# Kernel tuning notes

Hardware: AMD Instinct MI355X
Metric: run time of the kernel (lower is better)

## Reference

```python
import jax, jax.numpy as jnp
import numpy as np
from jax import lax

D_MODEL = 384
D_STATE = 16
D_CONV = 4
EXPAND = 2
D_INNER = EXPAND * D_MODEL            # 768
DT_RANK = int(np.ceil(D_INNER / 16))  # 48
B_SZ, L_SEQ = 8, 1024
LN_EPS = 1e-5


def setup_inputs() -> dict:
    key = jax.random.key(0)
    ks = jax.random.split(key, 10)
    x = jax.random.normal(ks[0], (B_SZ, L_SEQ, D_MODEL), dtype=jnp.float32)
    ln_g = jnp.ones((D_MODEL,), jnp.float32)
    ln_b = jnp.zeros((D_MODEL,), jnp.float32)
    in_proj_w = jax.random.normal(ks[1], (2 * D_INNER, D_MODEL), jnp.float32) * (D_MODEL ** -0.5)
    conv_w = jax.random.normal(ks[2], (D_INNER, 1, D_CONV), jnp.float32) * (D_CONV ** -0.5)
    conv_b = jax.random.normal(ks[3], (D_INNER,), jnp.float32) * 0.01
    x_proj_w = jax.random.normal(ks[4], (DT_RANK + 2 * D_STATE, D_INNER), jnp.float32) * (D_INNER ** -0.5)
    dt_std = DT_RANK ** -0.5
    dt_proj_w = jax.random.uniform(ks[5], (D_INNER, DT_RANK), jnp.float32, -dt_std, dt_std)
    dt_proj_b = jax.random.normal(ks[6], (D_INNER,), jnp.float32) * 0.01
    A_log = jnp.log(jnp.tile(jnp.arange(1, D_STATE + 1, dtype=jnp.float32), (D_INNER, 1)))
    D_param = jnp.ones((D_INNER,), jnp.float32)
    out_proj_w = jax.random.normal(ks[7], (D_MODEL, D_INNER), jnp.float32) * (D_INNER ** -0.5)
    return {"x": x, "ln_g": ln_g, "ln_b": ln_b, "in_proj_w": in_proj_w,
            "conv_w": conv_w, "conv_b": conv_b, "x_proj_w": x_proj_w,
            "dt_proj_w": dt_proj_w, "dt_proj_b": dt_proj_b, "A_log": A_log,
            "D_param": D_param, "out_proj_w": out_proj_w}


def _selective_scan(u, delta, A, Bm, Cm):
    # u, delta: (B,L,Din); A: (Din,N); Bm, Cm: (B,L,N)
    dA = jnp.exp(delta[..., None] * A)                 # (B,L,Din,N)
    dBu = (delta * u)[..., None] * Bm[:, :, None, :]   # (B,L,Din,N)
    dA_t = jnp.moveaxis(dA, 1, 0)                      # (L,B,Din,N)
    dBu_t = jnp.moveaxis(dBu, 1, 0)
    C_t = jnp.moveaxis(Cm, 1, 0)                       # (L,B,N)

    def step(h, inp):
        dA_s, dBu_s, c_s = inp
        h = dA_s * h + dBu_s                           # (B,Din,N)
        y = jnp.einsum('bdn,bn->bd', h, c_s)
        return h, y

    h0 = jnp.zeros((u.shape[0], u.shape[2], A.shape[1]), u.dtype)
    _, ys = lax.scan(step, h0, (dA_t, dBu_t, C_t))
    return jnp.moveaxis(ys, 0, 1)                      # (B,L,Din)


def reference(x, ln_g, ln_b, in_proj_w, conv_w, conv_b, x_proj_w,
              dt_proj_w, dt_proj_b, A_log, D_param, out_proj_w):
    residual = x
    # LayerNorm
    mu = jnp.mean(x, axis=-1, keepdims=True)
    var = jnp.var(x, axis=-1, keepdims=True)
    xn = (x - mu) * lax.rsqrt(var + LN_EPS) * ln_g + ln_b
    # in_proj and split
    xz = xn @ in_proj_w.T                              # (B,L,2*Din)
    xh, z = jnp.split(xz, 2, axis=-1)
    # causal depthwise conv1d (torch pads both sides then truncates to L)
    xc = lax.conv_general_dilated(
        jnp.moveaxis(xh, 1, 2), conv_w, (1,), [(D_CONV - 1, 0)],
        feature_group_count=D_INNER,
        dimension_numbers=('NCH', 'OIH', 'NCH')) + conv_b[None, :, None]
    u = jax.nn.silu(jnp.moveaxis(xc, 1, 2))            # (B,L,Din)
    # SSM input-dependent params
    xpo = u @ x_proj_w.T                               # (B,L,dt_rank+2N)
    dlow, Bm, Cm = jnp.split(xpo, [DT_RANK, DT_RANK + D_STATE], axis=-1)
    delta = jax.nn.softplus(dlow @ dt_proj_w.T + dt_proj_b)
    A = -jnp.exp(A_log)
    y = _selective_scan(u, delta, A, Bm, Cm)
    y = y + u * D_param
    y = y * jax.nn.silu(z)
    out = y @ out_proj_w.T
    return residual + out
```

## Files before the change

kernel.cpp:

```cpp
#include <hip/hip_runtime.h>
#include <math.h>

#define DMODEL 384
#define DIN 768
#define NST 16
#define DTR 48
#define BSZ 8
#define LSEQ 1024
#define NROWS (BSZ*LSEQ)
#define XPO_W (DTR + 2*NST)
#define CL 32
#define NC (LSEQ/CL)
#define CSEG 32

typedef __attribute__((ext_vector_type(8))) short bf16x8;
typedef __attribute__((ext_vector_type(4))) float f32x4;

__device__ __forceinline__ unsigned short f2bf(float x) {
  unsigned int u = __float_as_uint(x);
  unsigned int r = u + 0x7fffu + ((u >> 16) & 1u);
  return (unsigned short)(r >> 16);
}
__device__ __forceinline__ float bf2f(unsigned short h) {
  return __uint_as_float(((unsigned int)h) << 16);
}
__device__ __forceinline__ unsigned int pk2(float a, float b) {
  return (unsigned int)f2bf(a) | ((unsigned int)f2bf(b) << 16);
}

__device__ __forceinline__ void gll16(const void* g, void* l) {
  __builtin_amdgcn_global_load_lds(
      (const __attribute__((address_space(1))) void*)g,
      (__attribute__((address_space(3))) void*)l, 16, 0, 0);
}

__device__ __forceinline__ void split_one(const float* src, int ldsrc, int R, int C,
    unsigned short* dh, unsigned short* dl, int Cpad, int i) {
  int r = i / Cpad, c = i - r * Cpad;
  float v = (r < R && c < C) ? src[(size_t)r*ldsrc + c] : 0.f;
  unsigned short hv = f2bf(v);
  dh[i] = hv;
  dl[i] = f2bf(v - bf2f(hv));
}
#define N_INW (1536*384)
#define N_XW  (128*768)
#define N_DTW (768*64)
#define N_OW  (384*768)
#define NWBLK ((N_INW+N_XW+N_DTW+N_OW)/256)
__global__ __launch_bounds__(256) void prep_kernel(
    const float* __restrict__ inw, const float* __restrict__ xw,
    const float* __restrict__ dtw, const float* __restrict__ ow,
    unsigned short* inw_h, unsigned short* inw_l,
    unsigned short* xw_h, unsigned short* xw_l,
    unsigned short* dtw_h, unsigned short* dtw_l,
    unsigned short* ow_h, unsigned short* ow_l,
    const float* __restrict__ x, const float* __restrict__ g,
    const float* __restrict__ b,
    unsigned short* __restrict__ xh, unsigned short* __restrict__ xl) {
  if (blockIdx.x < NWBLK) {
    int i = blockIdx.x * 256 + threadIdx.x;
    if (i < N_INW) { split_one(inw, 384, 1536, 384, inw_h, inw_l, 384, i); return; }
    i -= N_INW;
    if (i < N_XW)  { split_one(xw, 768, 80, 768, xw_h, xw_l, 768, i); return; }
    i -= N_XW;
    if (i < N_DTW) { split_one(dtw, 48, 768, 48, dtw_h, dtw_l, 64, i); return; }
    i -= N_DTW;
    split_one(ow, 768, 384, 768, ow_h, ow_l, 768, i);
    return;
  }
  int row = (blockIdx.x - NWBLK) * 4 + (threadIdx.x >> 6);
  int lane = threadIdx.x & 63;
  const float* xr = x + (size_t)row * DMODEL;
  float v[6];
  float s = 0.f, ss = 0.f;
#pragma unroll
  for (int i = 0; i < 6; ++i) { v[i] = xr[lane + i*64]; s += v[i]; ss += v[i]*v[i]; }
#pragma unroll
  for (int off = 32; off; off >>= 1) { s += __shfl_xor(s, off); ss += __shfl_xor(ss, off); }
  float mu = s * (1.f / DMODEL);
  float var = ss * (1.f / DMODEL) - mu * mu;
  float inv = rsqrtf(var + 1e-5f);
#pragma unroll
  for (int i = 0; i < 6; ++i) {
    int c = lane + i*64;
    float o = (v[i] - mu) * inv * g[c] + b[c];
    unsigned short hv = f2bf(o);
    xh[(size_t)row*DMODEL + c] = hv;
    xl[(size_t)row*DMODEL + c] = f2bf(o - bf2f(hv));
  }
}

template<int EPI>
__global__ __launch_bounds__(256, 2) void gemm_mfma(
    const unsigned short* __restrict__ Ah, const unsigned short* __restrict__ Al, int lda,
    const unsigned short* __restrict__ Bh, const unsigned short* __restrict__ Bl, int ldb,
    float* __restrict__ C, int ldc, size_t strideS,
    const float* __restrict__ bias,
    int T) {
  __shared__ unsigned short lds[2][4][4096];
  int tid = threadIdx.x;
  int lane = tid & 63, wid = tid >> 6;
  int wm = wid >> 1, wn = wid & 1;

  unsigned nwg = gridDim.x * gridDim.y;
  unsigned bid = blockIdx.y * gridDim.x + blockIdx.x;
  unsigned cpx = nwg >> 3;
  unsigned sw = (bid & 7) * cpx + (bid >> 3);
  unsigned bx = sw % gridDim.x, by = sw / gridDim.x;
  int m0 = by * 128, n0 = bx * 128;
  C += (size_t)blockIdx.z * strideS;
  size_t kofs = (size_t)blockIdx.z * T * 32;

  f32x4 acc[4][4];
#pragma unroll
  for (int i = 0; i < 4; ++i)
#pragma unroll
    for (int j = 0; j < 4; ++j) acc[i][j] = (f32x4){0.f, 0.f, 0.f, 0.f};

  int kgl = lane >> 4, rl = lane & 15;

  int c0 = wid*128 + lane;
  int c1 = wid*128 + 64 + lane;
  int r0 = c0 & 127, kg0 = c0 >> 7;
  int r1 = c1 & 127, kg1 = c1 >> 7;

#define STAGE(bf, kt) do { \
    size_t ga0 = (size_t)(m0 + r0) * lda + (kt) + kg0*8 + kofs; \
    size_t gb0 = (size_t)(n0 + r0) * ldb + (kt) + kg0*8 + kofs; \
    size_t ga1 = (size_t)(m0 + r1) * lda + (kt) + kg1*8 + kofs; \
    size_t gb1 = (size_t)(n0 + r1) * ldb + (kt) + kg1*8 + kofs; \
    gll16(Ah + ga0, &lds[bf][0][(wid*128)*8]); \
    gll16(Al + ga0, &lds[bf][1][(wid*128)*8]); \
    gll16(Bh + gb0, &lds[bf][2][(wid*128)*8]); \
    gll16(Bl + gb0, &lds[bf][3][(wid*128)*8]); \
    gll16(Ah + ga1, &lds[bf][0][(wid*128+64)*8]); \
    gll16(Al + ga1, &lds[bf][1][(wid*128+64)*8]); \
    gll16(Bh + gb1, &lds[bf][2][(wid*128+64)*8]); \
    gll16(Bl + gb1, &lds[bf][3][(wid*128+64)*8]); \
  } while (0)

  STAGE(0, 0);
  asm volatile("s_waitcnt vmcnt(0)" ::: "memory");
  __builtin_amdgcn_s_barrier();

  int cur = 0;
  for (int t = 0; t < T; ++t) {
    if (t + 1 < T) {
      STAGE(cur ^ 1, (t + 1) << 5);
    }
    asm volatile("" ::: "memory");
    bf16x8 ah[4], al[4], bh[4], bl[4];
#pragma unroll
    for (int mi = 0; mi < 4; ++mi) {
      int cell = kgl*128 + wm*64 + mi*16 + rl;
      ah[mi] = *reinterpret_cast<const bf16x8*>(&lds[cur][0][cell*8]);
      al[mi] = *reinterpret_cast<const bf16x8*>(&lds[cur][1][cell*8]);
    }
#pragma unroll
    for (int ni = 0; ni < 4; ++ni) {
      int cell = kgl*128 + wn*64 + ni*16 + rl;
      bh[ni] = *reinterpret_cast<const bf16x8*>(&lds[cur][2][cell*8]);
      bl[ni] = *reinterpret_cast<const bf16x8*>(&lds[cur][3][cell*8]);
    }
#pragma unroll
    for (int mi = 0; mi < 4; ++mi)
#pragma unroll
      for (int ni = 0; ni < 4; ++ni) {
        acc[mi][ni] = __builtin_amdgcn_mfma_f32_16x16x32_bf16(ah[mi], bh[ni], acc[mi][ni], 0, 0, 0);
        acc[mi][ni] = __builtin_amdgcn_mfma_f32_16x16x32_bf16(al[mi], bh[ni], acc[mi][ni], 0, 0, 0);
        acc[mi][ni] = __builtin_amdgcn_mfma_f32_16x16x32_bf16(ah[mi], bl[ni], acc[mi][ni], 0, 0, 0);
      }
    asm volatile("s_waitcnt vmcnt(0)" ::: "memory");
    __builtin_amdgcn_s_barrier();
    cur ^= 1;
  }
#undef STAGE

#pragma unroll
  for (int mi = 0; mi < 4; ++mi)
#pragma unroll
    for (int ni = 0; ni < 4; ++ni)
#pragma unroll
      for (int j = 0; j < 4; ++j) {
        int m = m0 + wm*64 + mi*16 + (lane>>4)*4 + j;
        int n = n0 + wn*64 + ni*16 + (lane&15);
        float v = acc[mi][ni][j];
        if (EPI == 0) {
          C[(size_t)m*ldc + n] = v;
        } else if (EPI == 2) {
          v += bias[n];
          v = (v > 20.f) ? v : log1pf(__expf(v));
          C[(size_t)m*ldc + n] = v;
        }
      }
}

__global__ __launch_bounds__(256) void reduce_xproj(
    const float* __restrict__ P, float* __restrict__ xpo,
    unsigned short* __restrict__ dh, unsigned short* __restrict__ dl) {
  int idx = blockIdx.x * 256 + threadIdx.x;
  int m = idx >> 7, n = idx & 127;
  float v = 0.f;
#pragma unroll
  for (int s = 0; s < 4; ++s) v += P[(size_t)s * NROWS * 128 + idx];
  if (n < XPO_W) xpo[(size_t)m * XPO_W + n] = v;
  if (n < 64) {
    unsigned short hv = f2bf(v);
    dh[(size_t)m*64 + n] = hv;
    dl[(size_t)m*64 + n] = f2bf(v - bf2f(hv));
  }
}

__global__ __launch_bounds__(256) void reduce_out(
    const float* __restrict__ P, const float* __restrict__ x, float* __restrict__ out) {
  int i = blockIdx.x * 256 + threadIdx.x;
  const size_t S = (size_t)NROWS*DMODEL;
  out[i] = x[i] + ((P[i] + P[i + S]) + (P[i + 2*S] + P[i + 3*S]));
}

__global__ __launch_bounds__(256) void conv_silu_kernel(
    const float* __restrict__ xz, const float* __restrict__ w,
    const float* __restrict__ cb,
    unsigned short* __restrict__ uh, unsigned short* __restrict__ ul) {
  int d = blockIdx.x * 256 + threadIdx.x;
  int l0 = blockIdx.y * CSEG;
  int b = blockIdx.z;
  float xv[CSEG + 3];
#pragma unroll
  for (int i = 0; i < CSEG + 3; ++i) {
    int l = l0 + i - 3;
    xv[i] = (l >= 0) ? xz[((size_t)b*LSEQ + l) * (2*DIN) + d] : 0.f;
  }
  float w0 = w[d*4], w1 = w[d*4+1], w2 = w[d*4+2], w3 = w[d*4+3];
  float cbv = cb[d];
#pragma unroll
  for (int i = 0; i < CSEG; ++i) {
    float acc = cbv;
    acc = fmaf(xv[i],     w0, acc);
    acc = fmaf(xv[i + 1], w1, acc);
    acc = fmaf(xv[i + 2], w2, acc);
    acc = fmaf(xv[i + 3], w3, acc);
    float s = acc / (1.f + __expf(-acc));
    size_t idx = ((size_t)b*LSEQ + l0 + i) * DIN + d;
    unsigned short hv = f2bf(s);
    uh[idx] = hv;
    ul[idx] = f2bf(s - bf2f(hv));
  }
}

__global__ __launch_bounds__(256) void scan_pass1(
    const float* __restrict__ delta,
    const unsigned short* __restrict__ uh,
    const float* __restrict__ xpo, const float* __restrict__ A_log,
    unsigned short* __restrict__ carryA, unsigned short* __restrict__ carryH) {
  int d = blockIdx.x * 256 + threadIdx.x;
  int c = blockIdx.y, b = blockIdx.z;
  float A[16];
  {
    const float4* al = reinterpret_cast<const float4*>(A_log + (size_t)d * NST);
#pragma unroll
    for (int i = 0; i < 4; ++i) {
      float4 t = al[i];
      A[4*i+0] = -__expf(t.x); A[4*i+1] = -__expf(t.y);
      A[4*i+2] = -__expf(t.z); A[4*i+3] = -__expf(t.w);
    }
  }
  float h[16], ap[16];
#pragma unroll
  for (int n = 0; n < 16; ++n) { h[n] = 0.f; ap[n] = 1.f; }
  const float* dp = delta + ((size_t)b*LSEQ + c*CL) * DIN + d;
  const unsigned short* uhp = uh + ((size_t)b*LSEQ + c*CL) * DIN + d;
  const float* bp = xpo   + ((size_t)b*LSEQ + c*CL) * XPO_W + DTR;
  for (int l = 0; l < CL; ++l) {
    float dv = dp[(size_t)l*DIN];
    float uv = bf2f(uhp[(size_t)l*DIN]);
    float du = dv * uv;
    float Bv[16];
    {
      const float4* b4 = reinterpret_cast<const float4*>(bp + (size_t)l*XPO_W);
#pragma unroll
      for (int i = 0; i < 4; ++i) {
        float4 t = b4[i];
        Bv[4*i+0] = t.x; Bv[4*i+1] = t.y; Bv[4*i+2] = t.z; Bv[4*i+3] = t.w;
      }
    }
#pragma unroll
    for (int n = 0; n < 16; ++n) {
      float a = __expf(dv * A[n]);
      ap[n] *= a;
      h[n] = fmaf(a, h[n], du * Bv[n]);
    }
  }
  size_t ci = (((size_t)b*NC + c) * DIN + d) * NST;
  uint4* ca = reinterpret_cast<uint4*>(carryA + ci);
  uint4* ch = reinterpret_cast<uint4*>(carryH + ci);
  ca[0] = make_uint4(pk2(ap[0],ap[1]), pk2(ap[2],ap[3]), pk2(ap[4],ap[5]), pk2(ap[6],ap[7]));
  ca[1] = make_uint4(pk2(ap[8],ap[9]), pk2(ap[10],ap[11]), pk2(ap[12],ap[13]), pk2(ap[14],ap[15]));
  ch[0] = make_uint4(pk2(h[0],h[1]), pk2(h[2],h[3]), pk2(h[4],h[5]), pk2(h[6],h[7]));
  ch[1] = make_uint4(pk2(h[8],h[9]), pk2(h[10],h[11]), pk2(h[12],h[13]), pk2(h[14],h[15]));
}

__global__ __launch_bounds__(256) void scan_mid(
    const unsigned short* __restrict__ carryA, unsigned short* __restrict__ carryH) {
  int idx = blockIdx.x * 256 + threadIdx.x;
  int b = idx / (DIN*NST);
  int rem = idx - b * DIN*NST;
  float h = 0.f;
#pragma unroll
  for (int c = 0; c < NC; ++c) {
    size_t i = ((size_t)b*NC + c) * (DIN*NST) + rem;
    float a = bf2f(carryA[i]);
    float e = bf2f(carryH[i]);
    carryH[i] = f2bf(h);
    h = fmaf(a, h, e);
  }
}

__global__ __launch_bounds__(256) void scan_pass2(
    const float* __restrict__ delta,
    const unsigned short* __restrict__ uh,
    const float* __restrict__ xpo, const float* __restrict__ xz,
    const float* __restrict__ A_log, const float* __restrict__ Dp,
    const unsigned short* __restrict__ carryH,
    unsigned short* __restrict__ yh, unsigned short* __restrict__ yl) {
  int d = blockIdx.x * 256 + threadIdx.x;
  int c = blockIdx.y, b = blockIdx.z;
  float A[16];
  {
    const float4* al = reinterpret_cast<const float4*>(A_log + (size_t)d * NST);
#pragma unroll
    for (int i = 0; i < 4; ++i) {
      float4 t = al[i];
      A[4*i+0] = -__expf(t.x); A[4*i+1] = -__expf(t.y);
      A[4*i+2] = -__expf(t.z); A[4*i+3] = -__expf(t.w);
    }
  }
  float h[16];
  size_t ci = (((size_t)b*NC + c) * DIN + d) * NST;
  {
    const uint4* ch4 = reinterpret_cast<const uint4*>(carryH + ci);
    uint4 t0 = ch4[0], t1 = ch4[1];
    h[0] = bf2f(t0.x & 0xffff); h[1] = bf2f(t0.x >> 16);
    h[2] = bf2f(t0.y & 0xffff); h[3] = bf2f(t0.y >> 16);
    h[4] = bf2f(t0.z & 0xffff); h[5] = bf2f(t0.z >> 16);
    h[6] = bf2f(t0.w & 0xffff); h[7] = bf2f(t0.w >> 16);
    h[8] = bf2f(t1.x & 0xffff); h[9] = bf2f(t1.x >> 16);
    h[10] = bf2f(t1.y & 0xffff); h[11] = bf2f(t1.y >> 16);
    h[12] = bf2f(t1.z & 0xffff); h[13] = bf2f(t1.z >> 16);
    h[14] = bf2f(t1.w & 0xffff); h[15] = bf2f(t1.w >> 16);
  }
  float Dd = Dp[d];
  const float* dp = delta + ((size_t)b*LSEQ + c*CL) * DIN + d;
  const unsigned short* uhp = uh + ((size_t)b*LSEQ + c*CL) * DIN + d;
  const float* bp = xpo   + ((size_t)b*LSEQ + c*CL) * XPO_W + DTR;
  const float* zp = xz    + ((size_t)b*LSEQ + c*CL) * (2*DIN) + DIN + d;
  size_t yi0 = ((size_t)b*LSEQ + c*CL) * DIN + d;
  for (int l = 0; l < CL; ++l) {
    float dv = dp[(size_t)l*DIN];
    float uv = bf2f(uhp[(size_t)l*DIN]);
    float du = dv * uv;
    float Bv[16], Cv[16];
    {
      const float4* b4 = reinterpret_cast<const float4*>(bp + (size_t)l*XPO_W);
#pragma unroll
      for (int i = 0; i < 4; ++i) {
        float4 t = b4[i];
        Bv[4*i+0] = t.x; Bv[4*i+1] = t.y; Bv[4*i+2] = t.z; Bv[4*i+3] = t.w;
        float4 tc = b4[i+4];
        Cv[4*i+0] = tc.x; Cv[4*i+1] = tc.y; Cv[4*i+2] = tc.z; Cv[4*i+3] = tc.w;
      }
    }
    float p = 0.f;
#pragma unroll
    for (int n = 0; n < 16; ++n) {
      float a = __expf(dv * A[n]);
      h[n] = fmaf(a, h[n], du * Bv[n]);
      p = fmaf(h[n], Cv[n], p);
    }
    float z = zp[(size_t)l*(2*DIN)];
    float sz = z / (1.f + __expf(-z));
    float yv = fmaf(uv, Dd, p) * sz;
    unsigned short hv = f2bf(yv);
    yh[yi0 + (size_t)l*DIN] = hv;
    yl[yi0 + (size_t)l*DIN] = f2bf(yv - bf2f(hv));
  }
}

extern "C" void kernel_launch(void* const* d_in, const int* in_sizes, int n_in,
                              void* d_out, int out_size, void* d_ws, size_t ws_size,
                              hipStream_t stream) {
  const float* x          = (const float*)d_in[0];
  const float* ln_g       = (const float*)d_in[1];
  const float* ln_b       = (const float*)d_in[2];
  const float* in_proj_w  = (const float*)d_in[3];
  const float* conv_w     = (const float*)d_in[4];
  const float* conv_b     = (const float*)d_in[5];
  const float* x_proj_w   = (const float*)d_in[6];
  const float* dt_proj_w  = (const float*)d_in[7];
  const float* dt_proj_b  = (const float*)d_in[8];
  const float* A_log      = (const float*)d_in[9];
  const float* D_param    = (const float*)d_in[10];
  const float* out_proj_w = (const float*)d_in[11];

  char* w = (char*)d_ws;
  unsigned short* xn_h  = (unsigned short*)w;
  unsigned short* xn_l  = xn_h + (size_t)NROWS*DMODEL;
  unsigned short* dlow_h = (unsigned short*)w;
  unsigned short* dlow_l = dlow_h + (size_t)NROWS*64;
  unsigned short* carryA = (unsigned short*)w;
  unsigned short* carryH = carryA + (size_t)BSZ*NC*DIN*NST;
  char* p = w + (size_t)NROWS*DMODEL*4;
  float* xz = (float*)p;              p += (size_t)NROWS*2*DIN*4;
  unsigned short* u_h = (unsigned short*)p;
  unsigned short* u_l = u_h + (size_t)NROWS*DIN;      p += (size_t)NROWS*DIN*4;
  float* xpo = (float*)p;             p += (size_t)NROWS*XPO_W*4;
  float* delta = (float*)p;           p += (size_t)NROWS*DIN*4;
  unsigned short* inw_h = (unsigned short*)delta;
  unsigned short* inw_l = inw_h + (size_t)1536*384;
  unsigned short* xw_h  = inw_l + (size_t)1536*384;
  unsigned short* xw_l  = xw_h + (size_t)128*768;
  unsigned short* y2_h = (unsigned short*)p;
  unsigned short* y2_l = y2_h + (size_t)NROWS*DIN;
  float* xpart = (float*)p;           p += (size_t)NROWS*DIN*4;
  unsigned short* dtw_h = (unsigned short*)p;
  unsigned short* dtw_l = dtw_h + (size_t)768*64;
  unsigned short* ow_h  = dtw_l + (size_t)768*64;
  unsigned short* ow_l  = ow_h + (size_t)384*768;
  float* opart = xz;

  prep_kernel<<<NWBLK + NROWS/4, 256, 0, stream>>>(
      in_proj_w, x_proj_w, dt_proj_w, out_proj_w,
      inw_h, inw_l, xw_h, xw_l, dtw_h, dtw_l, ow_h, ow_l,
      x, ln_g, ln_b, xn_h, xn_l);

  gemm_mfma<0><<<dim3(12, 64, 1), 256, 0, stream>>>(xn_h, xn_l, DMODEL, inw_h, inw_l, DMODEL,
      xz, 2*DIN, 0, nullptr, 12);

  conv_silu_kernel<<<dim3(DIN/256, LSEQ/CSEG, BSZ), 256, 0, stream>>>(
      xz, conv_w, conv_b, u_h, u_l);

  gemm_mfma<0><<<dim3(1, 64, 4), 256, 0, stream>>>(u_h, u_l, DIN, xw_h, xw_l, DIN,
      xpart, 128, (size_t)NROWS*128, nullptr, 6);
  reduce_xproj<<<(NROWS*128)/256, 256, 0, stream>>>(xpart, xpo, dlow_h, dlow_l);

  gemm_mfma<2><<<dim3(6, 64, 1), 256, 0, stream>>>(dlow_h, dlow_l, 64, dtw_h, dtw_l, 64,
      delta, DIN, 0, dt_proj_b, 2);

  {
    dim3 g1(DIN/256, NC, BSZ);
    scan_pass1<<<g1, 256, 0, stream>>>(delta, u_h, xpo, A_log, carryA, carryH);
    scan_mid<<<(BSZ*DIN*NST)/256, 256, 0, stream>>>(carryA, carryH);
    scan_pass2<<<g1, 256, 0, stream>>>(delta, u_h, xpo, xz, A_log, D_param,
                                       carryH, y2_h, y2_l);
  }

  gemm_mfma<0><<<dim3(3, 64, 4), 256, 0, stream>>>(y2_h, y2_l, DIN, ow_h, ow_l, DIN,
      opart, DMODEL, (size_t)NROWS*DMODEL, nullptr, 6);
  reduce_out<<<(NROWS*DMODEL)/256, 256, 0, stream>>>(opart, x, (float*)d_out);
}
```

Baseline: 225.9 us.

## Replace split-K out_proj GEMM and reduction with 64x64 tile GEMM fusing residual

The out_proj GEMM previously ran as a split-K of 4 on 128x128 tiles, wrote four partial buffers, and needed a separate reduce kernel to sum them and add the residual. It now uses a dedicated 64x64-tile kernel with full K (24 steps of 32), double-buffered LDS staging, and a grid swizzle across 8 groups, and it adds the residual in the epilogue. This removes the partial-buffer traffic and one launch. The cost is less reuse per tile and a longer serial K loop per block.

```diff
diff --git a/kernel.cpp b/kernel.cpp
--- a/kernel.cpp
+++ b/kernel.cpp
@@ -195,6 +195,92 @@
       }
 }
 
+__global__ __launch_bounds__(256, 2) void gemm64_res(
+    const unsigned short* __restrict__ Ah, const unsigned short* __restrict__ Al, int lda,
+    const unsigned short* __restrict__ Bh, const unsigned short* __restrict__ Bl, int ldb,
+    float* __restrict__ C, int ldc,
+    const float* __restrict__ res, int T) {
+  __shared__ unsigned short lds[2][4][2048];
+  int tid = threadIdx.x;
+  int lane = tid & 63, wid = tid >> 6;
+  int wm = wid >> 1, wn = wid & 1;
+
+  unsigned nwg = gridDim.x * gridDim.y;
+  unsigned bid = blockIdx.y * gridDim.x + blockIdx.x;
+  unsigned cpx = nwg >> 3;
+  unsigned sw = (bid & 7) * cpx + (bid >> 3);
+  unsigned bx = sw % gridDim.x, by = sw / gridDim.x;
+  int m0 = by * 64, n0 = bx * 64;
+
+  f32x4 acc[2][2];
+#pragma unroll
+  for (int i = 0; i < 2; ++i)
+#pragma unroll
+    for (int j = 0; j < 2; ++j) acc[i][j] = (f32x4){0.f, 0.f, 0.f, 0.f};
+
+  int kgl = lane >> 4, rl = lane & 15;
+
+  int srow = tid & 63, skg = tid >> 6;
+  size_t ga = (size_t)(m0 + srow) * lda + skg * 8;
+  size_t gb = (size_t)(n0 + srow) * ldb + skg * 8;
+  int dst = tid * 8;
+
+#define STAGE64(bf, kt) do { \
+    gll16(Ah + ga + (kt), &lds[bf][0][dst]); \
+    gll16(Al + ga + (kt), &lds[bf][1][dst]); \
+    gll16(Bh + gb + (kt), &lds[bf][2][dst]); \
+    gll16(Bl + gb + (kt), &lds[bf][3][dst]); \
+  } while (0)
+
+  STAGE64(0, 0);
+  asm volatile("s_waitcnt vmcnt(0)" ::: "memory");
+  __builtin_amdgcn_s_barrier();
+
+  int cur = 0;
+  for (int t = 0; t < T; ++t) {
+    if (t + 1 < T) {
+      STAGE64(cur ^ 1, (t + 1) << 5);
+    }
+    asm volatile("" ::: "memory");
+    bf16x8 ah[2], al[2], bh[2], bl[2];
+#pragma unroll
+    for (int mi = 0; mi < 2; ++mi) {
+      int cell = kgl*64 + wm*32 + mi*16 + rl;
+      ah[mi] = *reinterpret_cast<const bf16x8*>(&lds[cur][0][cell*8]);
+      al[mi] = *reinterpret_cast<const bf16x8*>(&lds[cur][1][cell*8]);
+    }
+#pragma unroll
+    for (int ni = 0; ni < 2; ++ni) {
+      int cell = kgl*64 + wn*32 + ni*16 + rl;
+      bh[ni] = *reinterpret_cast<const bf16x8*>(&lds[cur][2][cell*8]);
+      bl[ni] = *reinterpret_cast<const bf16x8*>(&lds[cur][3][cell*8]);
+    }
+#pragma unroll
+    for (int mi = 0; mi < 2; ++mi)
+#pragma unroll
+      for (int ni = 0; ni < 2; ++ni) {
+        acc[mi][ni] = __builtin_amdgcn_mfma_f32_16x16x32_bf16(ah[mi], bh[ni], acc[mi][ni], 0, 0, 0);
+        acc[mi][ni] = __builtin_amdgcn_mfma_f32_16x16x32_bf16(al[mi], bh[ni], acc[mi][ni], 0, 0, 0);
+        acc[mi][ni] = __builtin_amdgcn_mfma_f32_16x16x32_bf16(ah[mi], bl[ni], acc[mi][ni], 0, 0, 0);
+      }
+    asm volatile("s_waitcnt vmcnt(0)" ::: "memory");
+    __builtin_amdgcn_s_barrier();
+    cur ^= 1;
+  }
+#undef STAGE64
+
+#pragma unroll
+  for (int mi = 0; mi < 2; ++mi)
+#pragma unroll
+    for (int ni = 0; ni < 2; ++ni)
+#pragma unroll
+      for (int j = 0; j < 4; ++j) {
+        int m = m0 + wm*32 + mi*16 + (lane>>4)*4 + j;
+        int n = n0 + wn*32 + ni*16 + rl;
+        C[(size_t)m*ldc + n] = acc[mi][ni][j] + res[(size_t)m*ldc + n];
+      }
+}
+
 __global__ __launch_bounds__(256) void reduce_xproj(
     const float* __restrict__ P, float* __restrict__ xpo,
     unsigned short* __restrict__ dh, unsigned short* __restrict__ dl) {
@@ -209,13 +295,6 @@
     dh[(size_t)m*64 + n] = hv;
     dl[(size_t)m*64 + n] = f2bf(v - bf2f(hv));
   }
-}
-
-__global__ __launch_bounds__(256) void reduce_out(
-    const float* __restrict__ P, const float* __restrict__ x, float* __restrict__ out) {
-  int i = blockIdx.x * 256 + threadIdx.x;
-  const size_t S = (size_t)NROWS*DMODEL;
-  out[i] = x[i] + ((P[i] + P[i + S]) + (P[i + 2*S] + P[i + 3*S]));
 }
 
 __global__ __launch_bounds__(256) void conv_silu_kernel(
@@ -426,7 +505,6 @@
   unsigned short* dtw_l = dtw_h + (size_t)768*64;
   unsigned short* ow_h  = dtw_l + (size_t)768*64;
   unsigned short* ow_l  = ow_h + (size_t)384*768;
-  float* opart = xz;
 
   prep_kernel<<<NWBLK + NROWS/4, 256, 0, stream>>>(
       in_proj_w, x_proj_w, dt_proj_w, out_proj_w,
@@ -454,7 +532,6 @@
                                        carryH, y2_h, y2_l);
   }
 
-  gemm_mfma<0><<<dim3(3, 64, 4), 256, 0, stream>>>(y2_h, y2_l, DIN, ow_h, ow_l, DIN,
-      opart, DMODEL, (size_t)NROWS*DMODEL, nullptr, 6);
-  reduce_out<<<(NROWS*DMODEL)/256, 256, 0, stream>>>(opart, x, (float*)d_out);
-}
+  gemm64_res<<<dim3(DMODEL/64, NROWS/64), 256, 0, stream>>>(y2_h, y2_l, DIN,
+      ow_h, ow_l, DIN, (float*)d_out, DMODEL, x, 24);
+}
```

Result: no change. 225.1 us (median of 2 runs) (-0.4%).
